# Optimization experiments

Measured on AMD Instinct MI355X. Metric: run time of the kernel, lower is better.

The kernel has to match this reference:

```python
import jax, jax.numpy as jnp
import numpy as np

B, T, I, H = 512, 49, 96, 1024  # batch, input_window_size-1, 3*nbones, hidden


def setup_inputs() -> dict:
    key = jax.random.key(0)
    k1, k2, k3, k4, k5 = jax.random.split(key, 5)
    s = 1.0 / np.sqrt(H)  # torch GRUCell init scale
    return {
        "enc_in": jax.random.normal(k1, (B, T, I), dtype=jnp.float32),
        "W_ih": jax.random.uniform(k2, (3 * H, I), jnp.float32, -s, s),
        "W_hh": jax.random.uniform(k3, (3 * H, H), jnp.float32, -s, s),
        "b_ih": jax.random.uniform(k4, (3 * H,), jnp.float32, -s, s),
        "b_hh": jax.random.uniform(k5, (3 * H,), jnp.float32, -s, s),
        "train": 1,
    }


def reference(enc_in, W_ih, W_hh, b_ih, b_hh, train):
    # Precompute input projections for all timesteps: [T, B, 3H]
    gi = jnp.einsum("bti,gi->tbg", enc_in, W_ih) + b_ih
    hdim = W_hh.shape[1]

    def step(h, gi_t):
        gh = h @ W_hh.T + b_hh                      # [B, 3H]
        ir, iz, inn = jnp.split(gi_t, 3, axis=-1)   # torch gate order: r, z, n
        hr, hz, hn = jnp.split(gh, 3, axis=-1)
        r = jax.nn.sigmoid(ir + hr)
        z = jax.nn.sigmoid(iz + hz)
        n = jnp.tanh(inn + r * hn)
        h_new = (1.0 - z) * n + z * h
        return h_new, None

    h0 = jnp.zeros((enc_in.shape[0], hdim), dtype=enc_in.dtype)
    h_last, _ = jax.lax.scan(step, h0, gi)
    return h_last  # enc_state: [B, H]
```

## Files before the change

kernel.cpp:

```cpp
#include <hip/hip_runtime.h>
#include <hip/hip_bf16.h>

#define B_ 512
#define T_ 49
#define I_ 96
#define H_ 1024

typedef __attribute__((ext_vector_type(4))) float f32x4;
typedef __attribute__((ext_vector_type(8))) short s16x8;

__device__ __forceinline__ unsigned short f2bf(float f) {
    unsigned int u = __float_as_uint(f);
    unsigned int r = (u + 0x7FFFu + ((u >> 16) & 1u)) >> 16;
    return (unsigned short)r;
}
__device__ __forceinline__ float sigmoidf_(float x) {
    return 1.0f / (1.0f + __expf(-x));
}
__device__ __forceinline__ float tanhf_(float x) {
    return 1.0f - 2.0f / (__expf(2.0f * x) + 1.0f);
}

__device__ __forceinline__ void gload_lds16(const unsigned short* g, unsigned short* l) {
    __builtin_amdgcn_global_load_lds(
        (const __attribute__((address_space(1))) void*)g,
        (__attribute__((address_space(3))) void*)l, 16, 0, 0);
}

__global__ void quantize_kernel(const float* __restrict__ Whh,
                                const float* __restrict__ Wih,
                                const float* __restrict__ x,
                                unsigned short* __restrict__ Whh_bf,
                                unsigned short* __restrict__ Wih_bf,
                                unsigned short* __restrict__ xT_bf) {
    const long stride = (long)gridDim.x * blockDim.x;
    const long idx = (long)blockIdx.x * blockDim.x + threadIdx.x;

    const long nWhh4 = (long)3 * H_ * H_ / 4;
    const long nWih4 = (long)3 * H_ * I_ / 4;
    const long nX4   = (long)B_ * T_ * I_ / 4;

    for (long i = idx; i < nWhh4; i += stride) {
        float4 v = ((const float4*)Whh)[i];
        ushort4 o; o.x = f2bf(v.x); o.y = f2bf(v.y); o.z = f2bf(v.z); o.w = f2bf(v.w);
        ((ushort4*)Whh_bf)[i] = o;
    }
    for (long i = idx; i < nWih4; i += stride) {
        float4 v = ((const float4*)Wih)[i];
        ushort4 o; o.x = f2bf(v.x); o.y = f2bf(v.y); o.z = f2bf(v.z); o.w = f2bf(v.w);
        ((ushort4*)Wih_bf)[i] = o;
    }
    for (long i = idx; i < nX4; i += stride) {
        float4 v = ((const float4*)x)[i];
        ushort4 o; o.x = f2bf(v.x); o.y = f2bf(v.y); o.z = f2bf(v.z); o.w = f2bf(v.w);
        const long e = i * 4;
        const int b  = (int)(e / (T_ * I_));
        const int rm = (int)(e - (long)b * (T_ * I_));
        const int tt = rm / I_;
        const int ii = rm - tt * I_;
        ((ushort4*)xT_bf)[(((long)tt * B_ + b) * I_ + ii) >> 2] = o;
    }
}

__global__ __launch_bounds__(512)
void gru_step3(const unsigned short* __restrict__ Whh_bf,
               const unsigned short* __restrict__ Wih_bf,
               const unsigned short* __restrict__ xT_bf,
               const float* __restrict__ b_ih,
               const float* __restrict__ b_hh,
               const float* __restrict__ h_in,
               const unsigned short* __restrict__ hbf_in,
               float* __restrict__ h_out,
               unsigned short* __restrict__ hbf_out,
               int t, int first)
{
    __shared__ __align__(16) unsigned short Wl[3 * 16 * 1024];
    __shared__ __align__(16) f32x4 Red[4 * 8 * 64];

    const int tid = threadIdx.x;
    const int w   = tid >> 6;
    const int l   = tid & 63;
    const int l15 = l & 15;
    const int l4  = l >> 4;
    const int mq  = w >> 1;
    const int kg  = w & 1;

    const int bid  = blockIdx.x;
    const int xcd  = bid & 7;
    const int r_   = bid >> 3;
    const int blkb = r_ & 3;
    const int blkj = xcd * 8 + (r_ >> 2);
    const int b0   = blkb * 128;
    const int j0   = blkj * 16;
    const int jg   = j0 + l15;
    const int brow = b0 + mq * 32;

    if (!first) {
#pragma unroll
        for (int i = 0; i < 12; ++i) {
            const int row  = w * 6 + (i >> 1);
            const int half = i & 1;
            const int g    = row >> 4;
            const int jj   = row & 15;
            const unsigned short* src = Whh_bf
                + ((long)g * H_ + j0 + jj) * H_ + half * 512
                + ((l ^ (jj & 7)) * 8);
            unsigned short* dst = Wl + (g * 16 + jj) * 1024 + half * 512;
            gload_lds16(src, dst);
        }
    }

    f32x4 accR[2], accZ[2], accNh[2], accNi[2];
#pragma unroll
    for (int m = 0; m < 2; ++m) {
        accR[m]  = (f32x4){0.f, 0.f, 0.f, 0.f};
        accZ[m]  = (f32x4){0.f, 0.f, 0.f, 0.f};
        accNh[m] = (f32x4){0.f, 0.f, 0.f, 0.f};
        accNi[m] = (f32x4){0.f, 0.f, 0.f, 0.f};
    }

    float hp[2][4] = {{0.f,0.f,0.f,0.f},{0.f,0.f,0.f,0.f}};
    if (kg == 0 && !first) {
#pragma unroll
        for (int f = 0; f < 2; ++f)
#pragma unroll
            for (int r = 0; r < 4; ++r)
                hp[f][r] = h_in[(long)(brow + f * 16 + l4 * 4 + r) * H_ + jg];
    }

    if (kg == 1) {
        const unsigned short* Ax0 = xT_bf + ((long)t * B_ + brow + l15) * I_ + l4 * 8;
        const unsigned short* Ax1 = Ax0 + 16 * I_;
        const unsigned short* Vr  = Wih_bf + (long)(j0 + l15) * I_ + l4 * 8;
        const unsigned short* Vz  = Wih_bf + (long)(H_ + j0 + l15) * I_ + l4 * 8;
        const unsigned short* Vn  = Wih_bf + (long)(2 * H_ + j0 + l15) * I_ + l4 * 8;
#pragma unroll
        for (int ks = 0; ks < 3; ++ks) {
            s16x8 a0 = *(const s16x8*)(Ax0 + ks * 32);
            s16x8 a1 = *(const s16x8*)(Ax1 + ks * 32);
            s16x8 br = *(const s16x8*)(Vr + ks * 32);
            s16x8 bz = *(const s16x8*)(Vz + ks * 32);
            s16x8 bn = *(const s16x8*)(Vn + ks * 32);
            accR[0]  = __builtin_amdgcn_mfma_f32_16x16x32_bf16(a0, br, accR[0], 0, 0, 0);
            accR[1]  = __builtin_amdgcn_mfma_f32_16x16x32_bf16(a1, br, accR[1], 0, 0, 0);
            accZ[0]  = __builtin_amdgcn_mfma_f32_16x16x32_bf16(a0, bz, accZ[0], 0, 0, 0);
            accZ[1]  = __builtin_amdgcn_mfma_f32_16x16x32_bf16(a1, bz, accZ[1], 0, 0, 0);
            accNi[0] = __builtin_amdgcn_mfma_f32_16x16x32_bf16(a0, bn, accNi[0], 0, 0, 0);
            accNi[1] = __builtin_amdgcn_mfma_f32_16x16x32_bf16(a1, bn, accNi[1], 0, 0, 0);
        }
    }

    if (!first) {
        const unsigned short* Ab0 = hbf_in + (long)(brow + l15) * H_ + kg * 512 + l4 * 8;
        const unsigned short* Ab1 = Ab0 + 16 * H_;
        const unsigned short* Wr  = Wl + (0 * 16 + l15) * 1024;
        const unsigned short* Wz  = Wl + (1 * 16 + l15) * 1024;
        const unsigned short* Wn  = Wl + (2 * 16 + l15) * 1024;
        const int swz   = (l15 & 7) << 3;
        const int kbase = kg * 512 + l4 * 8;

        s16x8 ring[3][4];

#pragma unroll
        for (int p = 0; p < 2; ++p) {
            ring[p][0] = *(const s16x8*)(Ab0 + p * 64);
            ring[p][1] = *(const s16x8*)(Ab0 + p * 64 + 32);
            ring[p][2] = *(const s16x8*)(Ab1 + p * 64);
            ring[p][3] = *(const s16x8*)(Ab1 + p * 64 + 32);
        }

        __syncthreads();

#pragma unroll
        for (int kk = 0; kk < 8; ++kk) {
            const int cur = kk % 3;
            const int nxt = (kk + 2) % 3;
            if (kk < 6) {
                ring[nxt][0] = *(const s16x8*)(Ab0 + (kk + 2) * 64);
                ring[nxt][1] = *(const s16x8*)(Ab0 + (kk + 2) * 64 + 32);
                ring[nxt][2] = *(const s16x8*)(Ab1 + (kk + 2) * 64);
                ring[nxt][3] = *(const s16x8*)(Ab1 + (kk + 2) * 64 + 32);
            }
#pragma unroll
            for (int q = 0; q < 2; ++q) {
                const int off = ((kbase + (kk * 2 + q) * 32) ^ swz);
                s16x8 br = *(const s16x8*)(Wr + off);
                s16x8 bz = *(const s16x8*)(Wz + off);
                s16x8 bn = *(const s16x8*)(Wn + off);
                s16x8 a0 = ring[cur][q * 1 + 0];
                s16x8 a1 = ring[cur][q * 1 + 2];
                accR[0]  = __builtin_amdgcn_mfma_f32_16x16x32_bf16(a0, br, accR[0], 0, 0, 0);
                accR[1]  = __builtin_amdgcn_mfma_f32_16x16x32_bf16(a1, br, accR[1], 0, 0, 0);
                accZ[0]  = __builtin_amdgcn_mfma_f32_16x16x32_bf16(a0, bz, accZ[0], 0, 0, 0);
                accZ[1]  = __builtin_amdgcn_mfma_f32_16x16x32_bf16(a1, bz, accZ[1], 0, 0, 0);
                accNh[0] = __builtin_amdgcn_mfma_f32_16x16x32_bf16(a0, bn, accNh[0], 0, 0, 0);
                accNh[1] = __builtin_amdgcn_mfma_f32_16x16x32_bf16(a1, bn, accNh[1], 0, 0, 0);
            }
        }
    }

    __syncthreads();
    if (kg == 1) {
        f32x4* dst = &Red[(mq * 8) * 64 + l];
        dst[0 * 64] = accR[0];  dst[1 * 64] = accR[1];
        dst[2 * 64] = accZ[0];  dst[3 * 64] = accZ[1];
        dst[4 * 64] = accNh[0]; dst[5 * 64] = accNh[1];
        dst[6 * 64] = accNi[0]; dst[7 * 64] = accNi[1];
    }
    __syncthreads();

    if (kg == 0) {
        const f32x4* srcp = &Red[(mq * 8) * 64 + l];
        accR[0]  += srcp[0 * 64]; accR[1]  += srcp[1 * 64];
        accZ[0]  += srcp[2 * 64]; accZ[1]  += srcp[3 * 64];
        accNh[0] += srcp[4 * 64]; accNh[1] += srcp[5 * 64];
        accNi[0] += srcp[6 * 64]; accNi[1] += srcp[7 * 64];

        const float bR   = b_ih[jg] + b_hh[jg];
        const float bZ   = b_ih[H_ + jg] + b_hh[H_ + jg];
        const float bihN = b_ih[2 * H_ + jg];
        const float bhhN = b_hh[2 * H_ + jg];

#pragma unroll
        for (int f = 0; f < 2; ++f) {
#pragma unroll
            for (int r = 0; r < 4; ++r) {
                const int row = brow + f * 16 + l4 * 4 + r;
                const long off = (long)row * H_ + jg;
                const float rg = sigmoidf_(accR[f][r] + bR);
                const float zg = sigmoidf_(accZ[f][r] + bZ);
                const float ng = tanhf_(accNi[f][r] + bihN + rg * (accNh[f][r] + bhhN));
                const float hn = (1.0f - zg) * ng + zg * hp[f][r];
                h_out[off] = hn;
                hbf_out[off] = f2bf(hn);
            }
        }
    }
}

extern "C" void kernel_launch(void* const* d_in, const int* in_sizes, int n_in,
                              void* d_out, int out_size, void* d_ws, size_t ws_size,
                              hipStream_t stream) {
    const float* enc_in = (const float*)d_in[0];
    const float* W_ih   = (const float*)d_in[1];
    const float* W_hh   = (const float*)d_in[2];
    const float* b_ih   = (const float*)d_in[3];
    const float* b_hh   = (const float*)d_in[4];
    float* out = (float*)d_out;

    char* ws = (char*)d_ws;
    unsigned short* Whh_bf = (unsigned short*)(ws);
    unsigned short* Wih_bf = (unsigned short*)(ws + 6291456);
    unsigned short* xT_bf  = (unsigned short*)(ws + 6881280);
    float* hA              = (float*)(ws + 11698176);
    float* hB              = (float*)(ws + 13795328);
    unsigned short* hbfA   = (unsigned short*)(ws + 15892480);
    unsigned short* hbfB   = (unsigned short*)(ws + 16941056);

    quantize_kernel<<<dim3(1024), dim3(256), 0, stream>>>(W_hh, W_ih, enc_in,
                                                          Whh_bf, Wih_bf, xT_bf);

    for (int t = 0; t < T_; ++t) {
        const int first = (t == 0) ? 1 : 0;
        float* hi; unsigned short* hbi; float* ho; unsigned short* hbo;
        if (t & 1) { hi = hA; hbi = hbfA; ho = hB; hbo = hbfB; }
        else       { hi = hB; hbi = hbfB; ho = hA; hbo = hbfA; }
        if (t == T_ - 1) ho = out;
        gru_step3<<<dim3(256), dim3(512), 0, stream>>>(Whh_bf, Wih_bf, xT_bf,
                                                       b_ih, b_hh, hi, hbi, ho, hbo,
                                                       t, first);
    }
}
```

Before: 734.3 us.

## Make GRU a persistent cooperative kernel with grid barriers across timesteps

Replaces the 49 per-timestep kernel launches with one cooperative persistent kernel. Each block loads its W_hh slice into LDS once, keeps the fp32 hidden state for its own tile in registers, and synchronises with other blocks through a per-timestep atomic counter grid barrier. This removes per-launch overhead and the repeated W_hh reload into LDS, and drops the fp32 hidden-state round trip through global memory. In exchange it adds spin-wait barrier latency, relies on all 256 blocks being co-resident, and preloads the whole h slice into registers instead of using a ring buffer, which raises register pressure.

```diff
diff --git a/kernel.cpp b/kernel.cpp
--- a/kernel.cpp
+++ b/kernel.cpp
@@ -5,6 +5,7 @@
 #define T_ 49
 #define I_ 96
 #define H_ 1024
+#define NBLK 256
 
 typedef __attribute__((ext_vector_type(4))) float f32x4;
 typedef __attribute__((ext_vector_type(8))) short s16x8;
@@ -32,9 +33,12 @@
                                 const float* __restrict__ x,
                                 unsigned short* __restrict__ Whh_bf,
                                 unsigned short* __restrict__ Wih_bf,
-                                unsigned short* __restrict__ xT_bf) {
+                                unsigned short* __restrict__ xT_bf,
+                                unsigned int* __restrict__ cnt) {
     const long stride = (long)gridDim.x * blockDim.x;
     const long idx = (long)blockIdx.x * blockDim.x + threadIdx.x;
+
+    if (blockIdx.x == 0 && threadIdx.x < T_) cnt[threadIdx.x] = 0;
 
     const long nWhh4 = (long)3 * H_ * H_ / 4;
     const long nWih4 = (long)3 * H_ * I_ / 4;
@@ -62,17 +66,16 @@
     }
 }
 
-__global__ __launch_bounds__(512)
-void gru_step3(const unsigned short* __restrict__ Whh_bf,
-               const unsigned short* __restrict__ Wih_bf,
-               const unsigned short* __restrict__ xT_bf,
-               const float* __restrict__ b_ih,
-               const float* __restrict__ b_hh,
-               const float* __restrict__ h_in,
-               const unsigned short* __restrict__ hbf_in,
-               float* __restrict__ h_out,
-               unsigned short* __restrict__ hbf_out,
-               int t, int first)
+__global__ __launch_bounds__(512, 2)
+void gru_persist2(const unsigned short* __restrict__ Whh_bf,
+                  const unsigned short* __restrict__ Wih_bf,
+                  const unsigned short* __restrict__ xT_bf,
+                  const float* __restrict__ b_ih,
+                  const float* __restrict__ b_hh,
+                  unsigned short* __restrict__ hbf0,
+                  unsigned short* __restrict__ hbf1,
+                  float* __restrict__ out,
+                  unsigned int* __restrict__ cnt)
 {
     __shared__ __align__(16) unsigned short Wl[3 * 16 * 1024];
     __shared__ __align__(16) f32x4 Red[4 * 8 * 64];
@@ -95,145 +98,145 @@
     const int jg   = j0 + l15;
     const int brow = b0 + mq * 32;
 
-    if (!first) {
-#pragma unroll
-        for (int i = 0; i < 12; ++i) {
-            const int row  = w * 6 + (i >> 1);
-            const int half = i & 1;
-            const int g    = row >> 4;
-            const int jj   = row & 15;
-            const unsigned short* src = Whh_bf
-                + ((long)g * H_ + j0 + jj) * H_ + half * 512
-                + ((l ^ (jj & 7)) * 8);
-            unsigned short* dst = Wl + (g * 16 + jj) * 1024 + half * 512;
-            gload_lds16(src, dst);
-        }
-    }
-
-    f32x4 accR[2], accZ[2], accNh[2], accNi[2];
-#pragma unroll
-    for (int m = 0; m < 2; ++m) {
-        accR[m]  = (f32x4){0.f, 0.f, 0.f, 0.f};
-        accZ[m]  = (f32x4){0.f, 0.f, 0.f, 0.f};
-        accNh[m] = (f32x4){0.f, 0.f, 0.f, 0.f};
-        accNi[m] = (f32x4){0.f, 0.f, 0.f, 0.f};
-    }
-
-    float hp[2][4] = {{0.f,0.f,0.f,0.f},{0.f,0.f,0.f,0.f}};
-    if (kg == 0 && !first) {
-#pragma unroll
-        for (int f = 0; f < 2; ++f)
-#pragma unroll
-            for (int r = 0; r < 4; ++r)
-                hp[f][r] = h_in[(long)(brow + f * 16 + l4 * 4 + r) * H_ + jg];
-    }
-
-    if (kg == 1) {
-        const unsigned short* Ax0 = xT_bf + ((long)t * B_ + brow + l15) * I_ + l4 * 8;
-        const unsigned short* Ax1 = Ax0 + 16 * I_;
-        const unsigned short* Vr  = Wih_bf + (long)(j0 + l15) * I_ + l4 * 8;
-        const unsigned short* Vz  = Wih_bf + (long)(H_ + j0 + l15) * I_ + l4 * 8;
-        const unsigned short* Vn  = Wih_bf + (long)(2 * H_ + j0 + l15) * I_ + l4 * 8;
-#pragma unroll
-        for (int ks = 0; ks < 3; ++ks) {
-            s16x8 a0 = *(const s16x8*)(Ax0 + ks * 32);
-            s16x8 a1 = *(const s16x8*)(Ax1 + ks * 32);
-            s16x8 br = *(const s16x8*)(Vr + ks * 32);
-            s16x8 bz = *(const s16x8*)(Vz + ks * 32);
-            s16x8 bn = *(const s16x8*)(Vn + ks * 32);
-            accR[0]  = __builtin_amdgcn_mfma_f32_16x16x32_bf16(a0, br, accR[0], 0, 0, 0);
-            accR[1]  = __builtin_amdgcn_mfma_f32_16x16x32_bf16(a1, br, accR[1], 0, 0, 0);
-            accZ[0]  = __builtin_amdgcn_mfma_f32_16x16x32_bf16(a0, bz, accZ[0], 0, 0, 0);
-            accZ[1]  = __builtin_amdgcn_mfma_f32_16x16x32_bf16(a1, bz, accZ[1], 0, 0, 0);
-            accNi[0] = __builtin_amdgcn_mfma_f32_16x16x32_bf16(a0, bn, accNi[0], 0, 0, 0);
-            accNi[1] = __builtin_amdgcn_mfma_f32_16x16x32_bf16(a1, bn, accNi[1], 0, 0, 0);
-        }
-    }
-
-    if (!first) {
-        const unsigned short* Ab0 = hbf_in + (long)(brow + l15) * H_ + kg * 512 + l4 * 8;
-        const unsigned short* Ab1 = Ab0 + 16 * H_;
-        const unsigned short* Wr  = Wl + (0 * 16 + l15) * 1024;
-        const unsigned short* Wz  = Wl + (1 * 16 + l15) * 1024;
-        const unsigned short* Wn  = Wl + (2 * 16 + l15) * 1024;
-        const int swz   = (l15 & 7) << 3;
-        const int kbase = kg * 512 + l4 * 8;
-
-        s16x8 ring[3][4];
-
-#pragma unroll
-        for (int p = 0; p < 2; ++p) {
-            ring[p][0] = *(const s16x8*)(Ab0 + p * 64);
-            ring[p][1] = *(const s16x8*)(Ab0 + p * 64 + 32);
-            ring[p][2] = *(const s16x8*)(Ab1 + p * 64);
-            ring[p][3] = *(const s16x8*)(Ab1 + p * 64 + 32);
-        }
-
-        __syncthreads();
-
-#pragma unroll
-        for (int kk = 0; kk < 8; ++kk) {
-            const int cur = kk % 3;
-            const int nxt = (kk + 2) % 3;
-            if (kk < 6) {
-                ring[nxt][0] = *(const s16x8*)(Ab0 + (kk + 2) * 64);
-                ring[nxt][1] = *(const s16x8*)(Ab0 + (kk + 2) * 64 + 32);
-                ring[nxt][2] = *(const s16x8*)(Ab1 + (kk + 2) * 64);
-                ring[nxt][3] = *(const s16x8*)(Ab1 + (kk + 2) * 64 + 32);
-            }
-#pragma unroll
-            for (int q = 0; q < 2; ++q) {
-                const int off = ((kbase + (kk * 2 + q) * 32) ^ swz);
-                s16x8 br = *(const s16x8*)(Wr + off);
-                s16x8 bz = *(const s16x8*)(Wz + off);
-                s16x8 bn = *(const s16x8*)(Wn + off);
-                s16x8 a0 = ring[cur][q * 1 + 0];
-                s16x8 a1 = ring[cur][q * 1 + 2];
+#pragma unroll
+    for (int i = 0; i < 12; ++i) {
+        const int row  = w * 6 + (i >> 1);
+        const int half = i & 1;
+        const int g    = row >> 4;
+        const int jj   = row & 15;
+        const unsigned short* src = Whh_bf
+            + ((long)g * H_ + j0 + jj) * H_ + half * 512
+            + ((l ^ (jj & 7)) * 8);
+        unsigned short* dst = Wl + (g * 16 + jj) * 1024 + half * 512;
+        gload_lds16(src, dst);
+    }
+
+    const float bR   = b_ih[jg] + b_hh[jg];
+    const float bZ   = b_ih[H_ + jg] + b_hh[H_ + jg];
+    const float bihN = b_ih[2 * H_ + jg];
+    const float bhhN = b_hh[2 * H_ + jg];
+
+    const unsigned short* Vr = Wih_bf + (long)(j0 + l15) * I_ + l4 * 8;
+    const unsigned short* Vz = Wih_bf + (long)(H_ + j0 + l15) * I_ + l4 * 8;
+    const unsigned short* Vn = Wih_bf + (long)(2 * H_ + j0 + l15) * I_ + l4 * 8;
+
+    const unsigned short* Wr = Wl + (0 * 16 + l15) * 1024;
+    const unsigned short* Wz = Wl + (1 * 16 + l15) * 1024;
+    const unsigned short* Wn = Wl + (2 * 16 + l15) * 1024;
+    const int swz   = (l15 & 7) << 3;
+    const int kbase = kg * 512 + l4 * 8;
+
+    float hreg[2][4] = {{0.f,0.f,0.f,0.f},{0.f,0.f,0.f,0.f}};
+
+    for (int t = 0; t < T_; ++t) {
+        const unsigned short* hin  = (t & 1) ? hbf1 : hbf0;
+        unsigned short*       hout = (t & 1) ? hbf0 : hbf1;
+
+        f32x4 accR[2], accZ[2], accNh[2], accNi[2];
+#pragma unroll
+        for (int m = 0; m < 2; ++m) {
+            accR[m]  = (f32x4){0.f, 0.f, 0.f, 0.f};
+            accZ[m]  = (f32x4){0.f, 0.f, 0.f, 0.f};
+            accNh[m] = (f32x4){0.f, 0.f, 0.f, 0.f};
+            accNi[m] = (f32x4){0.f, 0.f, 0.f, 0.f};
+        }
+
+        if (kg == 1) {
+            const unsigned short* Ax0 = xT_bf + ((long)t * B_ + brow + l15) * I_ + l4 * 8;
+            const unsigned short* Ax1 = Ax0 + 16 * I_;
+#pragma unroll
+            for (int ks = 0; ks < 3; ++ks) {
+                s16x8 a0 = *(const s16x8*)(Ax0 + ks * 32);
+                s16x8 a1 = *(const s16x8*)(Ax1 + ks * 32);
+                s16x8 br = *(const s16x8*)(Vr + ks * 32);
+                s16x8 bz = *(const s16x8*)(Vz + ks * 32);
+                s16x8 bn = *(const s16x8*)(Vn + ks * 32);
                 accR[0]  = __builtin_amdgcn_mfma_f32_16x16x32_bf16(a0, br, accR[0], 0, 0, 0);
                 accR[1]  = __builtin_amdgcn_mfma_f32_16x16x32_bf16(a1, br, accR[1], 0, 0, 0);
                 accZ[0]  = __builtin_amdgcn_mfma_f32_16x16x32_bf16(a0, bz, accZ[0], 0, 0, 0);
                 accZ[1]  = __builtin_amdgcn_mfma_f32_16x16x32_bf16(a1, bz, accZ[1], 0, 0, 0);
-                accNh[0] = __builtin_amdgcn_mfma_f32_16x16x32_bf16(a0, bn, accNh[0], 0, 0, 0);
-                accNh[1] = __builtin_amdgcn_mfma_f32_16x16x32_bf16(a1, bn, accNh[1], 0, 0, 0);
-            }
-        }
-    }
-
-    __syncthreads();
-    if (kg == 1) {
-        f32x4* dst = &Red[(mq * 8) * 64 + l];
-        dst[0 * 64] = accR[0];  dst[1 * 64] = accR[1];
-        dst[2 * 64] = accZ[0];  dst[3 * 64] = accZ[1];
-        dst[4 * 64] = accNh[0]; dst[5 * 64] = accNh[1];
-        dst[6 * 64] = accNi[0]; dst[7 * 64] = accNi[1];
-    }
-    __syncthreads();
-
-    if (kg == 0) {
-        const f32x4* srcp = &Red[(mq * 8) * 64 + l];
-        accR[0]  += srcp[0 * 64]; accR[1]  += srcp[1 * 64];
-        accZ[0]  += srcp[2 * 64]; accZ[1]  += srcp[3 * 64];
-        accNh[0] += srcp[4 * 64]; accNh[1] += srcp[5 * 64];
-        accNi[0] += srcp[6 * 64]; accNi[1] += srcp[7 * 64];
-
-        const float bR   = b_ih[jg] + b_hh[jg];
-        const float bZ   = b_ih[H_ + jg] + b_hh[H_ + jg];
-        const float bihN = b_ih[2 * H_ + jg];
-        const float bhhN = b_hh[2 * H_ + jg];
-
-#pragma unroll
-        for (int f = 0; f < 2; ++f) {
-#pragma unroll
-            for (int r = 0; r < 4; ++r) {
-                const int row = brow + f * 16 + l4 * 4 + r;
-                const long off = (long)row * H_ + jg;
-                const float rg = sigmoidf_(accR[f][r] + bR);
-                const float zg = sigmoidf_(accZ[f][r] + bZ);
-                const float ng = tanhf_(accNi[f][r] + bihN + rg * (accNh[f][r] + bhhN));
-                const float hn = (1.0f - zg) * ng + zg * hp[f][r];
-                h_out[off] = hn;
-                hbf_out[off] = f2bf(hn);
-            }
+                accNi[0] = __builtin_amdgcn_mfma_f32_16x16x32_bf16(a0, bn, accNi[0], 0, 0, 0);
+                accNi[1] = __builtin_amdgcn_mfma_f32_16x16x32_bf16(a1, bn, accNi[1], 0, 0, 0);
+            }
+        }
+
+        if (t > 0) {
+            const unsigned short* Ab0 = hin + (long)(brow + l15) * H_ + kg * 512 + l4 * 8;
+            const unsigned short* Ab1 = Ab0 + 16 * H_;
+
+            s16x8 Af[8][4];
+#pragma unroll
+            for (int kk = 0; kk < 8; ++kk) {
+                Af[kk][0] = *(const s16x8*)(Ab0 + kk * 64);
+                Af[kk][1] = *(const s16x8*)(Ab0 + kk * 64 + 32);
+                Af[kk][2] = *(const s16x8*)(Ab1 + kk * 64);
+                Af[kk][3] = *(const s16x8*)(Ab1 + kk * 64 + 32);
+            }
+
+#pragma unroll
+            for (int kk = 0; kk < 8; ++kk) {
+#pragma unroll
+                for (int q = 0; q < 2; ++q) {
+                    const int off = ((kbase + (kk * 2 + q) * 32) ^ swz);
+                    s16x8 br = *(const s16x8*)(Wr + off);
+                    s16x8 bz = *(const s16x8*)(Wz + off);
+                    s16x8 bn = *(const s16x8*)(Wn + off);
+                    s16x8 a0 = Af[kk][q];
+                    s16x8 a1 = Af[kk][q + 2];
+                    accR[0]  = __builtin_amdgcn_mfma_f32_16x16x32_bf16(a0, br, accR[0], 0, 0, 0);
+                    accR[1]  = __builtin_amdgcn_mfma_f32_16x16x32_bf16(a1, br, accR[1], 0, 0, 0);
+                    accZ[0]  = __builtin_amdgcn_mfma_f32_16x16x32_bf16(a0, bz, accZ[0], 0, 0, 0);
+                    accZ[1]  = __builtin_amdgcn_mfma_f32_16x16x32_bf16(a1, bz, accZ[1], 0, 0, 0);
+                    accNh[0] = __builtin_amdgcn_mfma_f32_16x16x32_bf16(a0, bn, accNh[0], 0, 0, 0);
+                    accNh[1] = __builtin_amdgcn_mfma_f32_16x16x32_bf16(a1, bn, accNh[1], 0, 0, 0);
+                }
+            }
+        }
+
+        __syncthreads();
+        if (kg == 1) {
+            f32x4* dst = &Red[(mq * 8) * 64 + l];
+            dst[0 * 64] = accR[0];  dst[1 * 64] = accR[1];
+            dst[2 * 64] = accZ[0];  dst[3 * 64] = accZ[1];
+            dst[4 * 64] = accNh[0]; dst[5 * 64] = accNh[1];
+            dst[6 * 64] = accNi[0]; dst[7 * 64] = accNi[1];
+        }
+        __syncthreads();
+
+        if (kg == 0) {
+            const f32x4* srcp = &Red[(mq * 8) * 64 + l];
+            accR[0]  += srcp[0 * 64]; accR[1]  += srcp[1 * 64];
+            accZ[0]  += srcp[2 * 64]; accZ[1]  += srcp[3 * 64];
+            accNh[0] += srcp[4 * 64]; accNh[1] += srcp[5 * 64];
+            accNi[0] += srcp[6 * 64]; accNi[1] += srcp[7 * 64];
+
+#pragma unroll
+            for (int f = 0; f < 2; ++f) {
+#pragma unroll
+                for (int r = 0; r < 4; ++r) {
+                    const float rg = sigmoidf_(accR[f][r] + bR);
+                    const float zg = sigmoidf_(accZ[f][r] + bZ);
+                    const float ng = tanhf_(accNi[f][r] + bihN + rg * (accNh[f][r] + bhhN));
+                    hreg[f][r] = (1.0f - zg) * ng + zg * hreg[f][r];
+                    const long off = (long)(brow + f * 16 + l4 * 4 + r) * H_ + jg;
+                    if (t < T_ - 1) hout[off] = f2bf(hreg[f][r]);
+                    else            out[off]  = hreg[f][r];
+                }
+            }
+        }
+
+        if (t < T_ - 1) {
+            __syncthreads();
+            if (tid == 0) {
+                __hip_atomic_fetch_add(&cnt[t], 1u, __ATOMIC_RELEASE,
+                                       __HIP_MEMORY_SCOPE_AGENT);
+                while (__hip_atomic_load(&cnt[t], __ATOMIC_RELAXED,
+                                         __HIP_MEMORY_SCOPE_AGENT) < NBLK)
+                    __builtin_amdgcn_s_sleep(2);
+                (void)__hip_atomic_load(&cnt[t], __ATOMIC_ACQUIRE,
+                                        __HIP_MEMORY_SCOPE_AGENT);
+            }
+            __syncthreads();
         }
     }
 }
@@ -252,22 +255,16 @@
     unsigned short* Whh_bf = (unsigned short*)(ws);
     unsigned short* Wih_bf = (unsigned short*)(ws + 6291456);
     unsigned short* xT_bf  = (unsigned short*)(ws + 6881280);
-    float* hA              = (float*)(ws + 11698176);
-    float* hB              = (float*)(ws + 13795328);
-    unsigned short* hbfA   = (unsigned short*)(ws + 15892480);
-    unsigned short* hbfB   = (unsigned short*)(ws + 16941056);
+    unsigned short* hbf0   = (unsigned short*)(ws + 11698176);
+    unsigned short* hbf1   = (unsigned short*)(ws + 12746752);
+    unsigned int*   cnt    = (unsigned int*)(ws + 13795328);
 
     quantize_kernel<<<dim3(1024), dim3(256), 0, stream>>>(W_hh, W_ih, enc_in,
-                                                          Whh_bf, Wih_bf, xT_bf);
-
-    for (int t = 0; t < T_; ++t) {
-        const int first = (t == 0) ? 1 : 0;
-        float* hi; unsigned short* hbi; float* ho; unsigned short* hbo;
-        if (t & 1) { hi = hA; hbi = hbfA; ho = hB; hbo = hbfB; }
-        else       { hi = hB; hbi = hbfB; ho = hA; hbo = hbfA; }
-        if (t == T_ - 1) ho = out;
-        gru_step3<<<dim3(256), dim3(512), 0, stream>>>(Whh_bf, Wih_bf, xT_bf,
-                                                       b_ih, b_hh, hi, hbi, ho, hbo,
-                                                       t, first);
-    }
-}
+                                                          Whh_bf, Wih_bf, xT_bf, cnt);
+
+    void* args[] = {(void*)&Whh_bf, (void*)&Wih_bf, (void*)&xT_bf,
+                    (void*)&b_ih, (void*)&b_hh,
+                    (void*)&hbf0, (void*)&hbf1, (void*)&out, (void*)&cnt};
+    hipLaunchCooperativeKernel((const void*)gru_persist2,
+                               dim3(256), dim3(512), args, 0, stream);
+}
```

Measured after the change: 1.143 ms. 1.56x slower.
